# Optimization experiments

Measured on AMD Instinct MI355X. Metric: run time of the kernel, lower is better.

## Reference

```python
import jax, jax.numpy as jnp
import numpy as np

E = 1024
H = 16
HD = 64
LN_EPS = 1e-5


def _layernorm(x, g, b):
    mu = jnp.mean(x, axis=-1, keepdims=True)
    var = jnp.mean((x - mu) ** 2, axis=-1, keepdims=True)
    return (x - mu) * jax.lax.rsqrt(var + LN_EPS) * g + b


def _positional(L):
    # PositionalEncoding: stepper = 1/10000^(arange(0,E,2)/E); cat(sin, cos) -> [L, E]
    stepper = 1.0 / (10000.0 ** (jnp.arange(0, E, 2, dtype=jnp.float32) / E))
    args = jnp.arange(L, dtype=jnp.float32)[:, None] * stepper[None, :]  # [L, E/2]
    return jnp.concatenate([jnp.sin(args), jnp.cos(args)], axis=1)  # [L, E]


def setup_inputs() -> dict:
    key = jax.random.key(0)
    ks = jax.random.split(key, 8)
    s = 1.0 / np.sqrt(E)
    return {
        "sequences": jax.random.normal(ks[0], (4, 2048, E), dtype=jnp.float32),
        "W_q": jax.random.normal(ks[1], (E, E), dtype=jnp.float32) * s,
        "W_k": jax.random.normal(ks[2], (E, E), dtype=jnp.float32) * s,
        "W_v": jax.random.normal(ks[3], (E, E), dtype=jnp.float32) * s,
        "W_o": jax.random.normal(ks[4], (E, E), dtype=jnp.float32) * s,
        "ln1_g": jnp.ones((E,), jnp.float32),
        "ln1_b": jnp.zeros((E,), jnp.float32),
        "lin_W": jax.random.normal(ks[5], (E, E), dtype=jnp.float32) * s,  # torch Linear weight [out,in]
        "lin_b": jnp.zeros((E,), jnp.float32),
        "ln2_g": jnp.ones((E,), jnp.float32),
        "ln2_b": jnp.zeros((E,), jnp.float32),
    }


def reference(sequences, W_q, W_k, W_v, W_o, ln1_g, ln1_b, lin_W, lin_b, ln2_g, ln2_b):
    B, L, _ = sequences.shape
    x = sequences + _positional(L)[None]  # add positional embeddings
    # projections (no bias)
    q = (x @ W_q).reshape(B, L, H, HD).transpose(0, 2, 1, 3)  # [B,H,L,hd]
    k = (x @ W_k).reshape(B, L, H, HD).transpose(0, 2, 1, 3)
    v = (x @ W_v).reshape(B, L, H, HD).transpose(0, 2, 1, 3)
    # linear (softmax-free) attention: (Q K^T / sqrt(hd)) V
    scores = jnp.einsum("bhqd,bhkd->bhqk", q, k) / jnp.sqrt(jnp.float32(HD))
    ctx = jnp.einsum("bhqk,bhkd->bhqd", scores, v)
    ctx = ctx.transpose(0, 2, 1, 3).reshape(B, L, E)
    attn_out = ctx @ W_o
    h = _layernorm(x + attn_out, ln1_g, ln1_b)
    ff = jax.nn.relu(h @ lin_W.T + lin_b)
    return _layernorm(ff + h, ln2_g, ln2_b)
```

## Files before the change

kernel.cpp:

```cpp
#include <hip/hip_runtime.h>
#include <cstdint>

typedef unsigned short u16;
typedef __bf16 bf16x8 __attribute__((ext_vector_type(8)));
typedef float f32x4 __attribute__((ext_vector_type(4)));

__device__ __forceinline__ u16 f2bf(float f) {
    unsigned u = __float_as_uint(f);
    u += 0x7fffu + ((u >> 16) & 1u);
    return (u16)(u >> 16);
}
__device__ __forceinline__ float bf2f(u16 h) {
    return __uint_as_float(((unsigned)h) << 16);
}

__device__ __forceinline__ void lds16(const void* g, void* l) {
    __builtin_amdgcn_global_load_lds(
        (const __attribute__((address_space(1))) void*)g,
        (__attribute__((address_space(3))) void*)l, 16, 0, 0);
}

__device__ __forceinline__ float pos_term(int l, int e) {
    const float c = -13.287712379549449f / 512.0f;
    int ii = e & 511;
    float st  = exp2f(c * (float)ii);
    float arg = (float)l * st;
    return (e < 512) ? sinf(arg) : cosf(arg);
}

__global__ __launch_bounds__(256) void prep_all(const float* __restrict__ seq,
                                                const float* __restrict__ wq,
                                                const float* __restrict__ wk,
                                                const float* __restrict__ wv,
                                                const float* __restrict__ wl,
                                                u16* __restrict__ xb,
                                                u16* __restrict__ wt) {
    const int bx = blockIdx.x;
    if (bx < 8192) {
        size_t i = (size_t)bx * 256 + threadIdx.x;
        int e4 = (int)(i & 255) * 4;
        int l  = (int)((i >> 8) & 2047);
        float4 s = ((const float4*)seq)[i];
        float v[4] = {s.x, s.y, s.z, s.w};
#pragma unroll
        for (int j = 0; j < 4; j++) v[j] += pos_term(l, e4 + j);
        ushort4 ob; ob.x = f2bf(v[0]); ob.y = f2bf(v[1]); ob.z = f2bf(v[2]); ob.w = f2bf(v[3]);
        ((ushort4*)xb)[i] = ob;
        return;
    }
    const int idx = bx - 8192;
    const int mat = idx >> 10, bxw = idx & 1023;
    const int gx = bxw & 31, gy = bxw >> 5;
    const int tx = threadIdx.x & 31, ty = threadIdx.x >> 5;
    const float* src = (mat == 0) ? wq : (mat == 1) ? wk : (mat == 2) ? wv : wl;
    u16* dst = wt + (size_t)mat * 1024 * 1024;
    if (mat == 0 || mat == 3) {
        int col = gx * 32 + tx, row0 = gy * 32;
#pragma unroll
        for (int j = 0; j < 32; j += 8)
            dst[(size_t)(row0 + ty + j) * 1024 + col] = f2bf(src[(size_t)(row0 + ty + j) * 1024 + col]);
    } else {
        __shared__ float tile[32][33];
        int col = gx * 32 + tx, row0 = gy * 32;
#pragma unroll
        for (int j = 0; j < 32; j += 8)
            tile[ty + j][tx] = src[(size_t)(row0 + ty + j) * 1024 + col];
        __syncthreads();
        int col2 = gy * 32 + tx, row20 = gx * 32;
#pragma unroll
        for (int j = 0; j < 32; j += 8)
            dst[(size_t)(row20 + ty + j) * 1024 + col2] = f2bf(tile[tx][ty + j]);
    }
}

__global__ __launch_bounds__(512) void gemm256(const u16* __restrict__ A,
                                               const u16* __restrict__ Bt,
                                               u16* __restrict__ C,
                                               int N, int K, int lda) {
    __shared__ __align__(16) u16 lds[65536];
    const int t = threadIdx.x;
    const int ntn = N >> 8;
    const int nwg = gridDim.x;
    int bid = (int)blockIdx.x;
    bid = (bid & 7) * (nwg >> 3) + (bid >> 3);
    const int tm = bid / ntn, tn = bid - tm * ntn;
    const size_t m0 = (size_t)tm << 8, n0 = (size_t)tn << 8;
    const int w = t >> 6, lane = t & 63;
    const int wr = w >> 2, wc = w & 3;

    const int r0 = t >> 3;
    const int ksrc = (t & 7) ^ (r0 & 7);
    const u16* sA0 = A + (m0 + r0) * (size_t)lda + ksrc * 8;
    const u16* sA1 = sA0 + (size_t)128 * lda;
    const u16* sB0 = Bt + (n0 + r0) * (size_t)K + ksrc * 8;
    const u16* sB1 = sB0 + (size_t)128 * K;
    const size_t stA = (size_t)64 * lda, stB = (size_t)64 * K;

#define STAGE(bb, hh, src, str, ko)                                           \
    do {                                                                      \
        u16* d_ = lds + (bb) * 32768 + (hh) * 8192 + (w << 9);                \
        lds16((src) + (ko), d_);                                              \
        lds16((src) + (ko) + (str), d_ + 4096);                               \
    } while (0)

    const int kx = lane & 7;
    const int ks0 = (((lane >> 4) ^ kx) << 3);
    const int ks1 = (((4 + (lane >> 4)) ^ kx) << 3);
    const int arow = (wr << 7) + (lane & 15);
    const int brow = (wc << 6) + (lane & 15);

    f32x4 acc[8][4];
#pragma unroll
    for (int i = 0; i < 8; i++)
#pragma unroll
        for (int j = 0; j < 4; j++)
#pragma unroll
            for (int r = 0; r < 4; r++) acc[i][j][r] = 0.0f;

    const int NT = K >> 6;
    STAGE(0, 0, sA0, stA, 0); STAGE(0, 1, sA1, stA, 0);
    STAGE(0, 2, sB0, stB, 0); STAGE(0, 3, sB1, stB, 0);

    for (int kt = 0; kt < NT; kt++) {
        const int b = kt & 1;
        const u16* Lb = lds + b * 32768;
        asm volatile("" ::: "memory");
        if (kt + 1 < NT) {
            const size_t ko = (size_t)(kt + 1) << 6;
            STAGE(b ^ 1, 0, sA0, stA, ko); STAGE(b ^ 1, 1, sA1, stA, ko);
            STAGE(b ^ 1, 2, sB0, stB, ko); STAGE(b ^ 1, 3, sB1, stB, ko);
            asm volatile("s_waitcnt vmcnt(8)" ::: "memory");
        } else {
            asm volatile("s_waitcnt vmcnt(0)" ::: "memory");
        }
        __builtin_amdgcn_s_barrier();
        asm volatile("" ::: "memory");

        bf16x8 af[4][2], b0[2][2], b1[2][2];
#pragma unroll
        for (int j = 0; j < 2; j++) {
            const int br = 16384 + ((brow + j * 16) << 6);
            b0[j][0] = *reinterpret_cast<const bf16x8*>(Lb + br + ks0);
            b0[j][1] = *reinterpret_cast<const bf16x8*>(Lb + br + ks1);
        }
#pragma unroll
        for (int j = 0; j < 2; j++) {
            const int br = 16384 + ((brow + 32 + j * 16) << 6);
            b1[j][0] = *reinterpret_cast<const bf16x8*>(Lb + br + ks0);
            b1[j][1] = *reinterpret_cast<const bf16x8*>(Lb + br + ks1);
        }
#pragma unroll
        for (int i = 0; i < 4; i++) {
            const int ar = (arow + i * 16) << 6;
            af[i][0] = *reinterpret_cast<const bf16x8*>(Lb + ar + ks0);
            af[i][1] = *reinterpret_cast<const bf16x8*>(Lb + ar + ks1);
        }
        __builtin_amdgcn_s_setprio(1);
#pragma unroll
        for (int kc = 0; kc < 2; kc++)
#pragma unroll
            for (int i = 0; i < 4; i++)
#pragma unroll
                for (int j = 0; j < 2; j++) {
                    acc[i][j] = __builtin_amdgcn_mfma_f32_16x16x32_bf16(
                        af[i][kc], b0[j][kc], acc[i][j], 0, 0, 0);
                    acc[i][2 + j] = __builtin_amdgcn_mfma_f32_16x16x32_bf16(
                        af[i][kc], b1[j][kc], acc[i][2 + j], 0, 0, 0);
                }
        __builtin_amdgcn_s_setprio(0);
#pragma unroll
        for (int i = 0; i < 4; i++) {
            const int ar = (arow + 64 + i * 16) << 6;
            af[i][0] = *reinterpret_cast<const bf16x8*>(Lb + ar + ks0);
            af[i][1] = *reinterpret_cast<const bf16x8*>(Lb + ar + ks1);
        }
        __builtin_amdgcn_s_setprio(1);
#pragma unroll
        for (int kc = 0; kc < 2; kc++)
#pragma unroll
            for (int i = 0; i < 4; i++)
#pragma unroll
                for (int j = 0; j < 2; j++) {
                    acc[4 + i][j] = __builtin_amdgcn_mfma_f32_16x16x32_bf16(
                        af[i][kc], b0[j][kc], acc[4 + i][j], 0, 0, 0);
                    acc[4 + i][2 + j] = __builtin_amdgcn_mfma_f32_16x16x32_bf16(
                        af[i][kc], b1[j][kc], acc[4 + i][2 + j], 0, 0, 0);
                }
        __builtin_amdgcn_s_setprio(0);
        asm volatile("" ::: "memory");
        __builtin_amdgcn_s_barrier();
    }
#undef STAGE

    const int crow = (lane >> 4) << 2, ccol = lane & 15;
#pragma unroll
    for (int i = 0; i < 8; i++)
#pragma unroll
        for (int j = 0; j < 4; j++) {
            size_t row = m0 + (wr << 7) + (i << 4) + crow;
            size_t col = n0 + (wc << 6) + (j << 4) + ccol;
#pragma unroll
            for (int r = 0; r < 4; r++)
                C[(row + r) * (size_t)N + col] = f2bf(acc[i][j][r]);
        }
}

template <int EPI>
__global__ __launch_bounds__(512) void gemm8p(const u16* __restrict__ A,
                                              const u16* __restrict__ Bt,
                                              void* __restrict__ Cv,
                                              const float* __restrict__ bias,
                                              int N, int K, int lda, size_t bstride) {
    __shared__ __align__(16) u16 lds[49152];
    const int t = threadIdx.x;
    const int ntn = N >> 8;
    const int nwg = gridDim.x;
    int bid = (int)blockIdx.x;
    bid = (bid & 7) * (nwg >> 3) + (bid >> 3);
    const int tm = bid / ntn, tn = bid - tm * ntn;
    const size_t m0 = (size_t)tm << 7, n0 = (size_t)tn << 8;
    const int w = t >> 6, lane = t & 63;
    const int wr = w >> 2, wc = w & 3;
    const u16* Bt_e = Bt + (bstride ? (m0 >> 11) * bstride : 0);

    const int r0 = t >> 3;
    const int ksrc = (t & 7) ^ (r0 & 7);
    const u16* sA0 = A + (m0 + r0) * (size_t)lda + ksrc * 8;
    const u16* sA1 = sA0 + (size_t)64 * lda;
    const u16* sB0 = Bt_e + (n0 + r0) * (size_t)K + ksrc * 8;
    const u16* sB1 = sB0 + (size_t)64 * K;
    const u16* sB2 = sB0 + (size_t)128 * K;
    const u16* sB3 = sB0 + (size_t)192 * K;
    u16* dstW = lds + (w << 9);

    const int ao = ((wr << 6) | (lane & 15)) << 6;
    const int bo = 8192 + ((((wc << 6) | (lane & 15))) << 6);
    const int kx = lane & 7;
    const int ks0 = (((lane >> 4) ^ kx) << 3);
    const int ks1 = (((4 + (lane >> 4)) ^ kx) << 3);

    f32x4 acc[4][4];
#pragma unroll
    for (int i = 0; i < 4; i++)
#pragma unroll
        for (int j = 0; j < 4; j++)
#pragma unroll
            for (int r = 0; r < 4; r++) acc[i][j][r] = 0.0f;

    const int NT = K >> 6;
    lds16(sA0, dstW);          lds16(sA1, dstW + 4096);
    lds16(sB0, dstW + 8192);   lds16(sB1, dstW + 12288);
    lds16(sB2, dstW + 16384);  lds16(sB3, dstW + 20480);

    for (int kt = 0; kt < NT; kt++) {
        const int b = kt & 1;
        asm volatile("" ::: "memory");
        if (kt + 1 < NT) {
            const size_t ko = (size_t)(kt + 1) << 6;
            u16* d = dstW + (b ^ 1) * 24576;
            lds16(sA0 + ko, d);          lds16(sA1 + ko, d + 4096);
            lds16(sB0 + ko, d + 8192);   lds16(sB1 + ko, d + 12288);
            lds16(sB2 + ko, d + 16384);  lds16(sB3 + ko, d + 20480);
            asm volatile("s_waitcnt vmcnt(6)" ::: "memory");
        } else {
            asm volatile("s_waitcnt vmcnt(0)" ::: "memory");
        }
        __builtin_amdgcn_s_barrier();
        asm volatile("" ::: "memory");
        const u16* Lb = lds + b * 24576;
#pragma unroll
        for (int kc = 0; kc < 2; kc++) {
            const int ksl = kc ? ks1 : ks0;
            bf16x8 af[4], bfr[4];
#pragma unroll
            for (int i = 0; i < 4; i++)
                af[i] = *reinterpret_cast<const bf16x8*>(Lb + ao + i * 1024 + ksl);
#pragma unroll
            for (int j = 0; j < 4; j++)
                bfr[j] = *reinterpret_cast<const bf16x8*>(Lb + bo + j * 1024 + ksl);
            __builtin_amdgcn_s_setprio(1);
#pragma unroll
            for (int i = 0; i < 4; i++)
#pragma unroll
                for (int j = 0; j < 4; j++)
                    acc[i][j] = __builtin_amdgcn_mfma_f32_16x16x32_bf16(af[i], bfr[j], acc[i][j], 0, 0, 0);
            __builtin_amdgcn_s_setprio(0);
        }
        asm volatile("" ::: "memory");
        __builtin_amdgcn_s_barrier();
    }

    const int crow = (lane >> 4) << 2, ccol = lane & 15;
#pragma unroll
    for (int i = 0; i < 4; i++)
#pragma unroll
        for (int j = 0; j < 4; j++) {
            size_t row = m0 + (wr << 6) + (i << 4) + crow;
            size_t col = n0 + (wc << 6) + (j << 4) + ccol;
#pragma unroll
            for (int r = 0; r < 4; r++) {
                float v = acc[i][j][r];
                if (EPI == 3) { v += bias[col]; v = fmaxf(v, 0.0f); }
                ((u16*)Cv)[(row + r) * (size_t)N + col] = f2bf(v);
            }
        }
}

template <bool ADDI>
__global__ __launch_bounds__(256) void gemm128(const u16* __restrict__ A,
                                               const u16* __restrict__ Bt,
                                               u16* __restrict__ C,
                                               int N, int K, int lda) {
    __shared__ __align__(16) u16 lds[32768];
    const int t = threadIdx.x;
    const int ntn = N >> 7;
    const int nwg = gridDim.x;
    int bid = (int)blockIdx.x;
    bid = (bid & 7) * (nwg >> 3) + (bid >> 3);
    const int tm = bid / ntn, tn = bid - tm * ntn;
    const size_t m0 = (size_t)tm << 7, n0 = (size_t)tn << 7;
    const int w = t >> 6, lane = t & 63;
    const int wr = w >> 1, wc = w & 1;

    const int r0 = t >> 3;
    const int ksrc = (t & 7) ^ (r0 & 7);
    const u16* sA = A + (m0 + r0) * (size_t)lda + ksrc * 8;
    const u16* sB = Bt + (n0 + r0) * (size_t)K + ksrc * 8;
    const size_t stA = (size_t)32 * lda, stB = (size_t)32 * K;

    const int kx = lane & 7;
    const int ks0 = (((lane >> 4) ^ kx) << 3);
    const int ks1 = (((4 + (lane >> 4)) ^ kx) << 3);
    const int ao = ((wr << 6) | (lane & 15)) << 6;
    const int bo = 8192 + ((((wc << 6) | (lane & 15))) << 6);

    f32x4 acc[4][4];
#pragma unroll
    for (int i = 0; i < 4; i++)
#pragma unroll
        for (int j = 0; j < 4; j++)
#pragma unroll
            for (int r = 0; r < 4; r++) acc[i][j][r] = 0.0f;

#define STAGE128(bb, ko)                                                      \
    do {                                                                      \
        u16* dA_ = lds + (bb) * 16384 + (w << 9);                             \
        u16* dB_ = dA_ + 8192;                                                \
        _Pragma("unroll")                                                     \
        for (int j_ = 0; j_ < 4; j_++) {                                      \
            lds16(sA + (ko) + j_ * stA, dA_ + j_ * 2048);                     \
            lds16(sB + (ko) + j_ * stB, dB_ + j_ * 2048);                     \
        }                                                                     \
    } while (0)

    const int NT = K >> 6;
    STAGE128(0, 0);
    for (int kt = 0; kt < NT; kt++) {
        const int b = kt & 1;
        asm volatile("" ::: "memory");
        if (kt + 1 < NT) {
            STAGE128(b ^ 1, (size_t)(kt + 1) << 6);
            asm volatile("s_waitcnt vmcnt(8)" ::: "memory");
        } else {
            asm volatile("s_waitcnt vmcnt(0)" ::: "memory");
        }
        __builtin_amdgcn_s_barrier();
        asm volatile("" ::: "memory");
        const u16* Lb = lds + b * 16384;
#pragma unroll
        for (int kc = 0; kc < 2; kc++) {
            const int ksl = kc ? ks1 : ks0;
            bf16x8 af[4], bfr[4];
#pragma unroll
            for (int i = 0; i < 4; i++)
                af[i] = *reinterpret_cast<const bf16x8*>(Lb + ao + i * 1024 + ksl);
#pragma unroll
            for (int j = 0; j < 4; j++)
                bfr[j] = *reinterpret_cast<const bf16x8*>(Lb + bo + j * 1024 + ksl);
            __builtin_amdgcn_s_setprio(1);
#pragma unroll
            for (int i = 0; i < 4; i++)
#pragma unroll
                for (int j = 0; j < 4; j++)
                    acc[i][j] = __builtin_amdgcn_mfma_f32_16x16x32_bf16(af[i], bfr[j], acc[i][j], 0, 0, 0);
            __builtin_amdgcn_s_setprio(0);
        }
        asm volatile("" ::: "memory");
        __builtin_amdgcn_s_barrier();
    }
#undef STAGE128

    const int crow = (lane >> 4) << 2, ccol = lane & 15;
#pragma unroll
    for (int i = 0; i < 4; i++)
#pragma unroll
        for (int j = 0; j < 4; j++) {
            size_t row = m0 + (wr << 6) + (i << 4) + crow;
            size_t col = n0 + (wc << 6) + (j << 4) + ccol;
#pragma unroll
            for (int r = 0; r < 4; r++) {
                float v = acc[i][j][r];
                if (ADDI && col == ((row + r) & 1023)) v += 1.0f;
                C[(row + r) * (size_t)N + col] = f2bf(v);
            }
        }
}

__global__ __launch_bounds__(256) void ktv_kernel(const u16* __restrict__ kv,
                                                  float* __restrict__ part) {
    const int bh = blockIdx.x, split = blockIdx.y;
    const int b = bh >> 4, h = bh & 15;
    const u16* Kp = kv + (size_t)b * 2048 * 2048 + h * 64;
    const u16* Vp = Kp + 1024;
    __shared__ float ks[8][64], vs[8][64];
    float acc[16];
#pragma unroll
    for (int i = 0; i < 16; i++) acc[i] = 0.0f;
    const int t = threadIdx.x, r = t >> 4, c = t & 15;
    const int lr = t >> 5, lc = (t & 31) * 2;
    for (int l0 = split * 128; l0 < split * 128 + 128; l0 += 8) {
        unsigned kk = *(const unsigned*)(Kp + (size_t)(l0 + lr) * 2048 + lc);
        unsigned vv = *(const unsigned*)(Vp + (size_t)(l0 + lr) * 2048 + lc);
        ks[lr][lc] = bf2f((u16)kk); ks[lr][lc + 1] = bf2f((u16)(kk >> 16));
        vs[lr][lc] = bf2f((u16)vv); vs[lr][lc + 1] = bf2f((u16)(vv >> 16));
        __syncthreads();
#pragma unroll
        for (int i = 0; i < 8; i++) {
            float kvr[4], vw[4];
#pragma unroll
            for (int a = 0; a < 4; a++) { kvr[a] = ks[i][r + 16 * a]; vw[a] = vs[i][c + 16 * a]; }
#pragma unroll
            for (int a = 0; a < 4; a++)
#pragma unroll
                for (int q = 0; q < 4; q++) acc[a * 4 + q] += kvr[a] * vw[q];
        }
        __syncthreads();
    }
    float* o = part + ((size_t)split * 64 + bh) * 4096;
#pragma unroll
    for (int a = 0; a < 4; a++)
#pragma unroll
        for (int q = 0; q < 4; q++) o[(r + 16 * a) * 64 + (c + 16 * q)] = acc[a * 4 + q];
}

__global__ __launch_bounds__(256) void ktv_reduce(const float* __restrict__ part,
                                                  float* __restrict__ ktv) {
    int i = blockIdx.x * 256 + threadIdx.x;
    float s = 0.0f;
#pragma unroll
    for (int sp = 0; sp < 16; sp++) s += part[(size_t)sp * 262144 + i];
    ktv[i] = s;
}

__global__ __launch_bounds__(256) void wprime_kernel(const float* __restrict__ ktv,
                                                     const float* __restrict__ Wo,
                                                     u16* __restrict__ wp) {
    const int n = blockIdx.x * 256 + threadIdx.x;
    const int h = blockIdx.y, b = blockIdx.z;
    const float* kt = ktv + ((size_t)(b * 16 + h) << 12);
    float acc[64];
#pragma unroll
    for (int i = 0; i < 64; i++) acc[i] = 0.0f;
    for (int j = 0; j < 64; j++) {
        float w = Wo[(size_t)(h * 64 + j) * 1024 + n];
#pragma unroll
        for (int i = 0; i < 64; i++) acc[i] += kt[i * 64 + j] * w;
    }
    u16* o = wp + ((size_t)b << 20) + (size_t)n * 1024 + h * 64;
    u16 ob[64];
#pragma unroll
    for (int i = 0; i < 64; i++) ob[i] = f2bf(acc[i] * 0.125f);
#pragma unroll
    for (int i = 0; i < 8; i++)
        ((uint4*)o)[i] = ((const uint4*)ob)[i];
}

__global__ __launch_bounds__(256) void ln1_kernel(const u16* __restrict__ xr,
                                                  const float* __restrict__ g,
                                                  const float* __restrict__ be,
                                                  u16* __restrict__ outB) {
    __shared__ float sm[4];
    const int row = blockIdx.x, t = threadIdx.x;
    const ushort4 xv = ((const ushort4*)(xr + (size_t)row * 1024))[t];
    float x0 = bf2f(xv.x), x1 = bf2f(xv.y), x2 = bf2f(xv.z), x3 = bf2f(xv.w);
    float s = x0 + x1 + x2 + x3;
#pragma unroll
    for (int off = 32; off > 0; off >>= 1) s += __shfl_down(s, off);
    if ((t & 63) == 0) sm[t >> 6] = s;
    __syncthreads();
    const float mean = (sm[0] + sm[1] + sm[2] + sm[3]) * (1.0f / 1024.0f);
    __syncthreads();
    x0 -= mean; x1 -= mean; x2 -= mean; x3 -= mean;
    float s2 = x0 * x0 + x1 * x1 + x2 * x2 + x3 * x3;
#pragma unroll
    for (int off = 32; off > 0; off >>= 1) s2 += __shfl_down(s2, off);
    if ((t & 63) == 0) sm[t >> 6] = s2;
    __syncthreads();
    const float var = (sm[0] + sm[1] + sm[2] + sm[3]) * (1.0f / 1024.0f);
    const float rs = rsqrtf(var + 1e-5f);
    const float4 gv = ((const float4*)g)[t];
    const float4 bv = ((const float4*)be)[t];
    ushort4 ob;
    ob.x = f2bf(x0 * rs * gv.x + bv.x);
    ob.y = f2bf(x1 * rs * gv.y + bv.y);
    ob.z = f2bf(x2 * rs * gv.z + bv.z);
    ob.w = f2bf(x3 * rs * gv.w + bv.w);
    ((ushort4*)(outB + (size_t)row * 1024))[t] = ob;
}

__global__ __launch_bounds__(256) void ln2_kernel(const u16* __restrict__ ff,
                                                  const u16* __restrict__ h1,
                                                  const float* __restrict__ g,
                                                  const float* __restrict__ be,
                                                  float* __restrict__ outF) {
    __shared__ float sm[4];
    const int row = blockIdx.x, t = threadIdx.x;
    const ushort4 fv = ((const ushort4*)(ff + (size_t)row * 1024))[t];
    const ushort4 hv = ((const ushort4*)(h1 + (size_t)row * 1024))[t];
    float x0 = bf2f(fv.x) + bf2f(hv.x), x1 = bf2f(fv.y) + bf2f(hv.y);
    float x2 = bf2f(fv.z) + bf2f(hv.z), x3 = bf2f(fv.w) + bf2f(hv.w);
    float s = x0 + x1 + x2 + x3;
#pragma unroll
    for (int off = 32; off > 0; off >>= 1) s += __shfl_down(s, off);
    if ((t & 63) == 0) sm[t >> 6] = s;
    __syncthreads();
    const float mean = (sm[0] + sm[1] + sm[2] + sm[3]) * (1.0f / 1024.0f);
    __syncthreads();
    x0 -= mean; x1 -= mean; x2 -= mean; x3 -= mean;
    float s2 = x0 * x0 + x1 * x1 + x2 * x2 + x3 * x3;
#pragma unroll
    for (int off = 32; off > 0; off >>= 1) s2 += __shfl_down(s2, off);
    if ((t & 63) == 0) sm[t >> 6] = s2;
    __syncthreads();
    const float var = (sm[0] + sm[1] + sm[2] + sm[3]) * (1.0f / 1024.0f);
    const float rs = rsqrtf(var + 1e-5f);
    const float4 gv = ((const float4*)g)[t];
    const float4 bv = ((const float4*)be)[t];
    float4 o;
    o.x = x0 * rs * gv.x + bv.x;
    o.y = x1 * rs * gv.y + bv.y;
    o.z = x2 * rs * gv.z + bv.z;
    o.w = x3 * rs * gv.w + bv.w;
    ((float4*)(outF + (size_t)row * 1024))[t] = o;
}

extern "C" void kernel_launch(void* const* d_in, const int* in_sizes, int n_in,
                              void* d_out, int out_size, void* d_ws, size_t ws_size,
                              hipStream_t stream) {
    const float* seq = (const float*)d_in[0];
    const float* Wq  = (const float*)d_in[1];
    const float* Wk  = (const float*)d_in[2];
    const float* Wv  = (const float*)d_in[3];
    const float* Wo  = (const float*)d_in[4];
    const float* g1  = (const float*)d_in[5];
    const float* b1  = (const float*)d_in[6];
    const float* Wl  = (const float*)d_in[7];
    const float* bl  = (const float*)d_in[8];
    const float* g2  = (const float*)d_in[9];
    const float* b2  = (const float*)d_in[10];

    char* ws = (char*)d_ws;
    const size_t MB = 1024 * 1024;
    u16*   x_bf    = (u16*)(ws + 0);
    u16*   wt      = (u16*)(ws + 16 * MB);
    u16*   kv      = (u16*)(ws + 24 * MB);
    float* kpart   = (float*)(ws + 56 * MB);
    u16*   attnres = (u16*)(ws + 56 * MB);
    float* ktv     = (float*)(ws + 72 * MB);
    u16*   wpr     = (u16*)(ws + 73 * MB);
    u16*   wcomb   = (u16*)(ws + 81 * MB);
    u16*   h1b     = (u16*)(ws + 89 * MB);
    u16*   ffb     = (u16*)(ws + 105 * MB);

    prep_all<<<dim3(8192 + 4096), dim3(256), 0, stream>>>(seq, Wq, Wk, Wv, Wl, x_bf, wt);
    gemm256<<<dim3(256), dim3(512), 0, stream>>>(x_bf, wt + (size_t)1 * MB, kv,
                                                 2048, 1024, 1024);
    ktv_kernel<<<dim3(64, 16), dim3(256), 0, stream>>>(kv, kpart);
    ktv_reduce<<<dim3(1024), dim3(256), 0, stream>>>(kpart, ktv);
    wprime_kernel<<<dim3(4, 16, 4), dim3(256), 0, stream>>>(ktv, Wo, wpr);
    gemm128<true><<<dim3(256), dim3(256), 0, stream>>>(wpr, wt, wcomb, 1024, 1024, 1024);
    gemm8p<2><<<dim3(256), dim3(512), 0, stream>>>(x_bf, wcomb, attnres, nullptr,
                                                   1024, 1024, 1024, (size_t)1024 * 1024);
    ln1_kernel<<<dim3(8192), dim3(256), 0, stream>>>(attnres, g1, b1, h1b);
    gemm8p<3><<<dim3(256), dim3(512), 0, stream>>>(h1b, wt + (size_t)3 * MB, ffb,
                                                   bl, 1024, 1024, 1024, 0);
    ln2_kernel<<<dim3(8192), dim3(256), 0, stream>>>(ffb, h1b, g2, b2, (float*)d_out);
}
```

Before: 190.6 us.

## Use 4-wave 256x256 GEMM with 128x128 per-wave tiles for K/V projection

The K/V projection GEMM changes from 8 waves (512 threads) computing 128x64 tiles each to 4 waves (256 threads) computing 128x128 tiles each. Each wave now holds a 8x8 grid of MFMA accumulators and loads 8 B fragments per k-chunk, which raises register reuse of LDS fragments. Each thread issues 16 global-to-LDS loads per stage. The trade-off is fewer waves per CU to hide latency and much higher register pressure (256 accumulator floats), which risks spills or lower overlap.

After: 196.2 us. 2.9% more time.

```diff
diff --git a/kernel.cpp b/kernel.cpp
--- a/kernel.cpp
+++ b/kernel.cpp
@@ -73,10 +73,10 @@
     }
 }
 
-__global__ __launch_bounds__(512) void gemm256(const u16* __restrict__ A,
-                                               const u16* __restrict__ Bt,
-                                               u16* __restrict__ C,
-                                               int N, int K, int lda) {
+__global__ __launch_bounds__(256, 1) void gemm256q(const u16* __restrict__ A,
+                                                   const u16* __restrict__ Bt,
+                                                   u16* __restrict__ C,
+                                                   int N, int K, int lda) {
     __shared__ __align__(16) u16 lds[65536];
     const int t = threadIdx.x;
     const int ntn = N >> 8;
@@ -86,119 +86,83 @@
     const int tm = bid / ntn, tn = bid - tm * ntn;
     const size_t m0 = (size_t)tm << 8, n0 = (size_t)tn << 8;
     const int w = t >> 6, lane = t & 63;
-    const int wr = w >> 2, wc = w & 3;
+    const int wr = w >> 1, wc = w & 1;
 
     const int r0 = t >> 3;
     const int ksrc = (t & 7) ^ (r0 & 7);
-    const u16* sA0 = A + (m0 + r0) * (size_t)lda + ksrc * 8;
-    const u16* sA1 = sA0 + (size_t)128 * lda;
-    const u16* sB0 = Bt + (n0 + r0) * (size_t)K + ksrc * 8;
-    const u16* sB1 = sB0 + (size_t)128 * K;
-    const size_t stA = (size_t)64 * lda, stB = (size_t)64 * K;
-
-#define STAGE(bb, hh, src, str, ko)                                           \
+    const u16* sA = A + (m0 + r0) * (size_t)lda + ksrc * 8;
+    const u16* sB = Bt + (n0 + r0) * (size_t)K + ksrc * 8;
+    const size_t stA = (size_t)32 * lda, stB = (size_t)32 * K;
+
+#define STAGEQ(bb, ko)                                                        \
     do {                                                                      \
-        u16* d_ = lds + (bb) * 32768 + (hh) * 8192 + (w << 9);                \
-        lds16((src) + (ko), d_);                                              \
-        lds16((src) + (ko) + (str), d_ + 4096);                               \
+        u16* d_ = lds + (bb) * 32768 + (w << 9);                              \
+        _Pragma("unroll")                                                     \
+        for (int k_ = 0; k_ < 8; k_++) {                                      \
+            lds16(sA + (ko) + k_ * stA, d_ + k_ * 2048);                      \
+            lds16(sB + (ko) + k_ * stB, d_ + 16384 + k_ * 2048);              \
+        }                                                                     \
     } while (0)
 
     const int kx = lane & 7;
     const int ks0 = (((lane >> 4) ^ kx) << 3);
     const int ks1 = (((4 + (lane >> 4)) ^ kx) << 3);
     const int arow = (wr << 7) + (lane & 15);
-    const int brow = (wc << 6) + (lane & 15);
-
-    f32x4 acc[8][4];
+    const int brow = (wc << 7) + (lane & 15);
+
+    f32x4 acc[8][8];
 #pragma unroll
     for (int i = 0; i < 8; i++)
 #pragma unroll
-        for (int j = 0; j < 4; j++)
+        for (int j = 0; j < 8; j++)
 #pragma unroll
             for (int r = 0; r < 4; r++) acc[i][j][r] = 0.0f;
 
     const int NT = K >> 6;
-    STAGE(0, 0, sA0, stA, 0); STAGE(0, 1, sA1, stA, 0);
-    STAGE(0, 2, sB0, stB, 0); STAGE(0, 3, sB1, stB, 0);
+    STAGEQ(0, 0);
 
     for (int kt = 0; kt < NT; kt++) {
         const int b = kt & 1;
         const u16* Lb = lds + b * 32768;
         asm volatile("" ::: "memory");
         if (kt + 1 < NT) {
-            const size_t ko = (size_t)(kt + 1) << 6;
-            STAGE(b ^ 1, 0, sA0, stA, ko); STAGE(b ^ 1, 1, sA1, stA, ko);
-            STAGE(b ^ 1, 2, sB0, stB, ko); STAGE(b ^ 1, 3, sB1, stB, ko);
-            asm volatile("s_waitcnt vmcnt(8)" ::: "memory");
+            STAGEQ(b ^ 1, (size_t)(kt + 1) << 6);
+            asm volatile("s_waitcnt vmcnt(16)" ::: "memory");
         } else {
             asm volatile("s_waitcnt vmcnt(0)" ::: "memory");
         }
         __builtin_amdgcn_s_barrier();
         asm volatile("" ::: "memory");
 
-        bf16x8 af[4][2], b0[2][2], b1[2][2];
-#pragma unroll
-        for (int j = 0; j < 2; j++) {
-            const int br = 16384 + ((brow + j * 16) << 6);
-            b0[j][0] = *reinterpret_cast<const bf16x8*>(Lb + br + ks0);
-            b0[j][1] = *reinterpret_cast<const bf16x8*>(Lb + br + ks1);
-        }
-#pragma unroll
-        for (int j = 0; j < 2; j++) {
-            const int br = 16384 + ((brow + 32 + j * 16) << 6);
-            b1[j][0] = *reinterpret_cast<const bf16x8*>(Lb + br + ks0);
-            b1[j][1] = *reinterpret_cast<const bf16x8*>(Lb + br + ks1);
-        }
-#pragma unroll
-        for (int i = 0; i < 4; i++) {
-            const int ar = (arow + i * 16) << 6;
-            af[i][0] = *reinterpret_cast<const bf16x8*>(Lb + ar + ks0);
-            af[i][1] = *reinterpret_cast<const bf16x8*>(Lb + ar + ks1);
-        }
-        __builtin_amdgcn_s_setprio(1);
-#pragma unroll
-        for (int kc = 0; kc < 2; kc++)
-#pragma unroll
-            for (int i = 0; i < 4; i++)
-#pragma unroll
-                for (int j = 0; j < 2; j++) {
-                    acc[i][j] = __builtin_amdgcn_mfma_f32_16x16x32_bf16(
-                        af[i][kc], b0[j][kc], acc[i][j], 0, 0, 0);
-                    acc[i][2 + j] = __builtin_amdgcn_mfma_f32_16x16x32_bf16(
-                        af[i][kc], b1[j][kc], acc[i][2 + j], 0, 0, 0);
-                }
-        __builtin_amdgcn_s_setprio(0);
-#pragma unroll
-        for (int i = 0; i < 4; i++) {
-            const int ar = (arow + 64 + i * 16) << 6;
-            af[i][0] = *reinterpret_cast<const bf16x8*>(Lb + ar + ks0);
-            af[i][1] = *reinterpret_cast<const bf16x8*>(Lb + ar + ks1);
-        }
-        __builtin_amdgcn_s_setprio(1);
-#pragma unroll
-        for (int kc = 0; kc < 2; kc++)
-#pragma unroll
-            for (int i = 0; i < 4; i++)
-#pragma unroll
-                for (int j = 0; j < 2; j++) {
-                    acc[4 + i][j] = __builtin_amdgcn_mfma_f32_16x16x32_bf16(
-                        af[i][kc], b0[j][kc], acc[4 + i][j], 0, 0, 0);
-                    acc[4 + i][2 + j] = __builtin_amdgcn_mfma_f32_16x16x32_bf16(
-                        af[i][kc], b1[j][kc], acc[4 + i][2 + j], 0, 0, 0);
-                }
-        __builtin_amdgcn_s_setprio(0);
+#pragma unroll
+        for (int kc = 0; kc < 2; kc++) {
+            const int ksl = kc ? ks1 : ks0;
+            bf16x8 bfr[8];
+#pragma unroll
+            for (int j = 0; j < 8; j++)
+                bfr[j] = *reinterpret_cast<const bf16x8*>(Lb + 16384 + ((brow + j * 16) << 6) + ksl);
+            __builtin_amdgcn_s_setprio(1);
+#pragma unroll
+            for (int i = 0; i < 8; i++) {
+                const bf16x8 af = *reinterpret_cast<const bf16x8*>(Lb + ((arow + i * 16) << 6) + ksl);
+#pragma unroll
+                for (int j = 0; j < 8; j++)
+                    acc[i][j] = __builtin_amdgcn_mfma_f32_16x16x32_bf16(af, bfr[j], acc[i][j], 0, 0, 0);
+            }
+            __builtin_amdgcn_s_setprio(0);
+        }
         asm volatile("" ::: "memory");
         __builtin_amdgcn_s_barrier();
     }
-#undef STAGE
+#undef STAGEQ
 
     const int crow = (lane >> 4) << 2, ccol = lane & 15;
 #pragma unroll
     for (int i = 0; i < 8; i++)
 #pragma unroll
-        for (int j = 0; j < 4; j++) {
+        for (int j = 0; j < 8; j++) {
             size_t row = m0 + (wr << 7) + (i << 4) + crow;
-            size_t col = n0 + (wc << 6) + (j << 4) + ccol;
+            size_t col = n0 + (wc << 7) + (j << 4) + ccol;
 #pragma unroll
             for (int r = 0; r < 4; r++)
                 C[(row + r) * (size_t)N + col] = f2bf(acc[i][j][r]);
@@ -573,8 +537,8 @@
     u16*   ffb     = (u16*)(ws + 105 * MB);
 
     prep_all<<<dim3(8192 + 4096), dim3(256), 0, stream>>>(seq, Wq, Wk, Wv, Wl, x_bf, wt);
-    gemm256<<<dim3(256), dim3(512), 0, stream>>>(x_bf, wt + (size_t)1 * MB, kv,
-                                                 2048, 1024, 1024);
+    gemm256q<<<dim3(256), dim3(256), 0, stream>>>(x_bf, wt + (size_t)1 * MB, kv,
+                                                  2048, 1024, 1024);
     ktv_kernel<<<dim3(64, 16), dim3(256), 0, stream>>>(kv, kpart);
     ktv_reduce<<<dim3(1024), dim3(256), 0, stream>>>(kpart, ktv);
     wprime_kernel<<<dim3(4, 16, 4), dim3(256), 0, stream>>>(ktv, Wo, wpr);
```
